# Kernel tuning notes

Hardware: AMD Instinct MI355X
Metric: run time of the kernel (lower is better)

Reference implementation:

```python
import jax, jax.numpy as jnp
import numpy as np

B = 64            # number of graphs
NODES_PER_G = 64  # real nodes per graph
N_MAX = 128       # max_num_nodes (dense padding)
NT = B * NODES_PER_G   # 4096 total nodes
E = 65536         # edges (and pairs)
H = 64            # hidden_dim
D_NODE = 32
POLY = 16


def setup_inputs() -> dict:
    key = jax.random.key(0)
    ks = jax.random.split(key, 12)
    node_x = jax.random.normal(ks[0], (NT, D_NODE), dtype=jnp.float32)
    loop_x = jax.random.normal(ks[1], (NT, POLY), dtype=jnp.float32)
    edge_attr = jax.random.normal(ks[2], (E, D_NODE), dtype=jnp.float32)
    pair_x = jax.random.normal(ks[3], (E, POLY), dtype=jnp.float32)
    W_node = jax.random.normal(ks[4], (D_NODE, H), dtype=jnp.float32) / np.sqrt(D_NODE)
    W_loop = jax.random.normal(ks[5], (POLY, H), dtype=jnp.float32) / np.sqrt(POLY)
    W_edge = jax.random.normal(ks[6], (D_NODE, H), dtype=jnp.float32) / np.sqrt(D_NODE)
    W_pair = jax.random.normal(ks[7], (POLY, H), dtype=jnp.float32) / np.sqrt(POLY)
    # sorted graph assignment: 64 nodes per graph
    batch = (jnp.arange(NT, dtype=jnp.int32) // NODES_PER_G).astype(jnp.int32)
    # intra-graph edges: global index = graph*NODES_PER_G + local
    epg = E // B  # edges per graph
    eg = (jnp.arange(E, dtype=jnp.int32) // epg)
    e_loc = jax.random.randint(ks[8], (2, E), 0, NODES_PER_G, dtype=jnp.int32)
    edge_index = eg[None, :] * NODES_PER_G + e_loc
    p_loc = jax.random.randint(ks[9], (2, E), 0, NODES_PER_G, dtype=jnp.int32)
    pair_index = eg[None, :] * NODES_PER_G + p_loc
    return {
        "node_x": node_x, "loop_x": loop_x, "edge_attr": edge_attr, "pair_x": pair_x,
        "W_node": W_node, "W_loop": W_loop, "W_edge": W_edge, "W_pair": W_pair,
        "batch": batch, "edge_index": edge_index, "pair_index": pair_index,
    }


def _positions(batch):
    # position of each node within its graph (to_dense_batch semantics)
    counts = jax.ops.segment_sum(jnp.ones_like(batch), batch, num_segments=B)
    starts = jnp.concatenate([jnp.zeros((1,), counts.dtype), jnp.cumsum(counts)[:-1]])
    return jnp.arange(batch.shape[0], dtype=batch.dtype) - starts[batch].astype(batch.dtype)


def _to_dense_adj(index, batch, pos, h):
    b = batch[index[0]]
    r = pos[index[0]]
    c = pos[index[1]]
    dense = jnp.zeros((B, N_MAX, N_MAX, H), dtype=h.dtype)
    return dense.at[b, r, c].add(h)  # duplicates are summed, as in to_dense_adj


def reference(node_x, loop_x, edge_attr, pair_x, W_node, W_loop, W_edge, W_pair,
              batch, edge_index, pair_index):
    pos = _positions(batch)
    # node + loop encoders (linear), then scatter to dense batch [B, N, H]
    node_h = node_x @ W_node + loop_x @ W_loop
    dense_node_h = jnp.zeros((B, N_MAX, H), dtype=node_h.dtype).at[batch, pos].set(node_h)
    dense_node_mask = jnp.zeros((B, N_MAX), dtype=bool).at[batch, pos].set(True)
    # permute (0,2,1) -> [B, H, N], then diag_embed -> [B, H, N, N]
    dnh = jnp.transpose(dense_node_h, (0, 2, 1))
    ar = jnp.arange(N_MAX)
    dense_diag_h = jnp.zeros((B, H, N_MAX, N_MAX), dtype=dnh.dtype).at[:, :, ar, ar].set(dnh)
    # edge + pair encoders, scatter to dense adjacency [B, N, N, H]
    edge_h = edge_attr @ W_edge
    pair_h = pair_x @ W_pair
    dense_pair = _to_dense_adj(edge_index, batch, pos, edge_h) \
               + _to_dense_adj(pair_index, batch, pos, pair_h)
    # permute (0,3,1,2) -> [B, H, N, N], add diagonal node features
    dense_pair_h = jnp.transpose(dense_pair, (0, 3, 1, 2)) + dense_diag_h
    return dense_pair_h, dense_node_mask
```

## Files before the change

### kernel.cpp

```cpp
#include <hip/hip_runtime.h>

#define NTOT  4096
#define NG    64
#define NMAXD 128
#define HD    64
#define NEDGE 65536
#define EPG   (NEDGE / NG)
#define NPG   (NTOT / NG)

typedef float f4 __attribute__((ext_vector_type(4)));

__global__ __launch_bounds__(1024) void prep_kernel(const int* __restrict__ batch,
                                                    int* __restrict__ starts,
                                                    int* __restrict__ pos,
                                                    int* __restrict__ counts) {
  const int tid = threadIdx.x;
  for (int i = tid; i < NTOT; i += 1024)
    if (i == 0 || batch[i] != batch[i - 1]) starts[batch[i]] = i;
  if (tid == 0) starts[NG] = NTOT;
  __syncthreads();
  for (int i = tid; i < NTOT; i += 1024) pos[i] = i - starts[batch[i]];
  if (tid < NG) counts[tid] = starts[tid + 1] - starts[tid];
}

#define HQ 4
#define SCT 512
__global__ __launch_bounds__(SCT) void fused_scatter_kernel(
    const float* __restrict__ node_x, const float* __restrict__ loop_x,
    const float* __restrict__ edge_attr, const float* __restrict__ pair_x,
    const float* __restrict__ Wn, const float* __restrict__ Wl,
    const float* __restrict__ We, const float* __restrict__ Wp,
    const int* __restrict__ eI, const int* __restrict__ pI,
    const int* __restrict__ batch, const int* __restrict__ pos,
    const int* __restrict__ counts,
    float* __restrict__ out, float* __restrict__ mask) {
  __shared__ float acc[HQ * 4096];
  __shared__ f4 WcE[32];
  __shared__ f4 WcP[16];
  __shared__ f4 WcN[48];

  const int tid = threadIdx.x;
  const int d  = (int)blockIdx.x;
  const int g  = ((d & 7) << 3) | ((d >> 3) & 7);
  const int h0 = (d >> 6) * HQ;

  if (tid < 32)       WcE[tid]            = *(const f4*)&We[tid * HD + h0];
  else if (tid < 48)  WcP[tid - 32]       = *(const f4*)&Wp[(tid - 32) * HD + h0];
  else if (tid < 80)  WcN[tid - 48]       = *(const f4*)&Wn[(tid - 48) * HD + h0];
  else if (tid < 96)  WcN[32 + tid - 80]  = *(const f4*)&Wl[(tid - 80) * HD + h0];
  for (int i = tid; i < HQ * 1024; i += SCT) ((f4*)acc)[i] = (f4)(0.f);
  __syncthreads();

  const int wid = tid >> 6;
  if (wid >= 4) {
    const int tz = tid - 256;
#pragma unroll
    for (int t = 0; t < HQ; ++t) {
      f4* plane = (f4*)(out + ((size_t)g * HD + h0 + t) * NMAXD * NMAXD);
#pragma unroll
      for (int k = 0; k < 4; ++k) {
        const int idx = tz + k * 256;
        const int r = idx >> 4, c4 = 16 + (idx & 15);
        plane[r * 32 + c4] = (f4)(0.f);
      }
#pragma unroll
      for (int k = 0; k < 8; ++k)
        plane[2048 + tz + k * 256] = (f4)(0.f);
    }
    if (h0 == 0) {
      const int cg = counts[g];
      for (int i = tz; i < NMAXD; i += 256)
        mask[(size_t)g * NMAXD + i] = (i < cg) ? 1.0f : 0.0f;
    }
  } else {
    const int la = tid;

    for (int jj = la; jj < EPG; jj += 256) {
      const int j = g * EPG + jj;
      const f4* xr = (const f4*)(edge_attr + (size_t)j * 32);
      f4 d4 = (f4)(0.f);
#pragma unroll
      for (int k4 = 0; k4 < 8; ++k4) {
        const f4 x = xr[k4];
#pragma unroll
        for (int u = 0; u < 4; ++u) d4 += x[u] * WcE[k4 * 4 + u];
      }
      const int n0 = eI[j], n1 = eI[NEDGE + j];
      const int b = batch[n0], r = pos[n0], c = pos[n1];
      if (b == g && r < 64 && c < 64) {
        const int a = r * 64 + c;
        atomicAdd(&acc[a], d4.x);          atomicAdd(&acc[4096 + a], d4.y);
        atomicAdd(&acc[8192 + a], d4.z);   atomicAdd(&acc[12288 + a], d4.w);
      } else {
        atomicAdd(&out[(((size_t)b * HD + h0 + 0) * NMAXD + r) * NMAXD + c], d4.x);
        atomicAdd(&out[(((size_t)b * HD + h0 + 1) * NMAXD + r) * NMAXD + c], d4.y);
        atomicAdd(&out[(((size_t)b * HD + h0 + 2) * NMAXD + r) * NMAXD + c], d4.z);
        atomicAdd(&out[(((size_t)b * HD + h0 + 3) * NMAXD + r) * NMAXD + c], d4.w);
      }
    }

    for (int jj = la; jj < EPG; jj += 256) {
      const int j = g * EPG + jj;
      const f4* xr = (const f4*)(pair_x + (size_t)j * 16);
      f4 d4 = (f4)(0.f);
#pragma unroll
      for (int k4 = 0; k4 < 4; ++k4) {
        const f4 x = xr[k4];
#pragma unroll
        for (int u = 0; u < 4; ++u) d4 += x[u] * WcP[k4 * 4 + u];
      }
      const int n0 = pI[j], n1 = pI[NEDGE + j];
      const int b = batch[n0], r = pos[n0], c = pos[n1];
      if (b == g && r < 64 && c < 64) {
        const int a = r * 64 + c;
        atomicAdd(&acc[a], d4.x);          atomicAdd(&acc[4096 + a], d4.y);
        atomicAdd(&acc[8192 + a], d4.z);   atomicAdd(&acc[12288 + a], d4.w);
      } else {
        atomicAdd(&out[(((size_t)b * HD + h0 + 0) * NMAXD + r) * NMAXD + c], d4.x);
        atomicAdd(&out[(((size_t)b * HD + h0 + 1) * NMAXD + r) * NMAXD + c], d4.y);
        atomicAdd(&out[(((size_t)b * HD + h0 + 2) * NMAXD + r) * NMAXD + c], d4.z);
        atomicAdd(&out[(((size_t)b * HD + h0 + 3) * NMAXD + r) * NMAXD + c], d4.w);
      }
    }

    for (int jj = la; jj < NPG; jj += 256) {
      const int j = g * NPG + jj;
      const f4* xr = (const f4*)(node_x + (size_t)j * 32);
      const f4* lr = (const f4*)(loop_x + (size_t)j * 16);
      f4 d4 = (f4)(0.f);
#pragma unroll
      for (int k4 = 0; k4 < 8; ++k4) {
        const f4 x = xr[k4];
#pragma unroll
        for (int u = 0; u < 4; ++u) d4 += x[u] * WcN[k4 * 4 + u];
      }
#pragma unroll
      for (int k4 = 0; k4 < 4; ++k4) {
        const f4 x = lr[k4];
#pragma unroll
        for (int u = 0; u < 4; ++u) d4 += x[u] * WcN[32 + k4 * 4 + u];
      }
      const int b = batch[j], r = pos[j];
      if (b == g && r < 64) {
        const int a = r * 64 + r;
        atomicAdd(&acc[a], d4.x);          atomicAdd(&acc[4096 + a], d4.y);
        atomicAdd(&acc[8192 + a], d4.z);   atomicAdd(&acc[12288 + a], d4.w);
      } else {
        atomicAdd(&out[(((size_t)b * HD + h0 + 0) * NMAXD + r) * NMAXD + r], d4.x);
        atomicAdd(&out[(((size_t)b * HD + h0 + 1) * NMAXD + r) * NMAXD + r], d4.y);
        atomicAdd(&out[(((size_t)b * HD + h0 + 2) * NMAXD + r) * NMAXD + r], d4.z);
        atomicAdd(&out[(((size_t)b * HD + h0 + 3) * NMAXD + r) * NMAXD + r], d4.w);
      }
    }
  }
  __syncthreads();

#pragma unroll
  for (int t = 0; t < HQ; ++t) {
    f4* plane = (f4*)(out + ((size_t)g * HD + h0 + t) * NMAXD * NMAXD);
#pragma unroll
    for (int k = 0; k < 2; ++k) {
      const int idx = tid + k * SCT;
      const int r = idx >> 4, c4 = idx & 15;
      plane[r * 32 + c4] = *(const f4*)&acc[t * 4096 + r * 64 + c4 * 4];
    }
  }
}

extern "C" void kernel_launch(void* const* d_in, const int* in_sizes, int n_in,
                              void* d_out, int out_size, void* d_ws, size_t ws_size,
                              hipStream_t stream) {
  const float* node_x    = (const float*)d_in[0];
  const float* loop_x    = (const float*)d_in[1];
  const float* edge_attr = (const float*)d_in[2];
  const float* pair_x    = (const float*)d_in[3];
  const float* W_node    = (const float*)d_in[4];
  const float* W_loop    = (const float*)d_in[5];
  const float* W_edge    = (const float*)d_in[6];
  const float* W_pair    = (const float*)d_in[7];
  const int*   batch     = (const int*)d_in[8];
  const int*   edge_index = (const int*)d_in[9];
  const int*   pair_index = (const int*)d_in[10];

  float* out  = (float*)d_out;
  float* mask = out + (size_t)NG * HD * NMAXD * NMAXD;

  int* pos    = (int*)d_ws;
  int* starts = pos + NTOT;
  int* counts = starts + (NG + 1);

  prep_kernel<<<1, 1024, 0, stream>>>(batch, starts, pos, counts);
  fused_scatter_kernel<<<NG * 16, SCT, 0, stream>>>(node_x, loop_x, edge_attr,
      pair_x, W_node, W_loop, W_edge, W_pair, edge_index, pair_index,
      batch, pos, counts, out, mask);
}
```

Baseline: 91.68 us.

## Split zero-fill into separate blocks so all scatter threads process edges

```diff
diff --git a/kernel.cpp b/kernel.cpp
--- a/kernel.cpp
+++ b/kernel.cpp
@@ -23,9 +23,12 @@
   if (tid < NG) counts[tid] = starts[tid + 1] - starts[tid];
 }
 
-#define HQ 4
-#define SCT 512
-__global__ __launch_bounds__(SCT) void fused_scatter_kernel(
+#define HQ  4
+#define BT  512
+#define NBB 1024
+#define NZB 1024
+
+__global__ __launch_bounds__(BT) void mega_kernel(
     const float* __restrict__ node_x, const float* __restrict__ loop_x,
     const float* __restrict__ edge_attr, const float* __restrict__ pair_x,
     const float* __restrict__ Wn, const float* __restrict__ Wl,
@@ -34,12 +37,29 @@
     const int* __restrict__ batch, const int* __restrict__ pos,
     const int* __restrict__ counts,
     float* __restrict__ out, float* __restrict__ mask) {
+  const int tid = threadIdx.x;
+
+  if ((int)blockIdx.x >= NBB) {
+    const int z = (int)blockIdx.x - NBB;
+#pragma unroll
+    for (int t = 0; t < 4; ++t) {
+      f4* plane = (f4*)(out + (size_t)(z * 4 + t) * (NMAXD * NMAXD));
+#pragma unroll
+      for (int k = 0; k < 4; ++k) plane[2048 + tid + k * BT] = (f4)(0.f);
+#pragma unroll
+      for (int k = 0; k < 2; ++k) {
+        const int i = tid + k * BT;
+        plane[(i >> 4) * 32 + 16 + (i & 15)] = (f4)(0.f);
+      }
+    }
+    return;
+  }
+
   __shared__ float acc[HQ * 4096];
   __shared__ f4 WcE[32];
   __shared__ f4 WcP[16];
   __shared__ f4 WcN[48];
 
-  const int tid = threadIdx.x;
   const int d  = (int)blockIdx.x;
   const int g  = ((d & 7) << 3) | ((d >> 3) & 7);
   const int h0 = (d >> 6) * HQ;
@@ -48,109 +68,84 @@
   else if (tid < 48)  WcP[tid - 32]       = *(const f4*)&Wp[(tid - 32) * HD + h0];
   else if (tid < 80)  WcN[tid - 48]       = *(const f4*)&Wn[(tid - 48) * HD + h0];
   else if (tid < 96)  WcN[32 + tid - 80]  = *(const f4*)&Wl[(tid - 80) * HD + h0];
-  for (int i = tid; i < HQ * 1024; i += SCT) ((f4*)acc)[i] = (f4)(0.f);
+  for (int i = tid; i < HQ * 1024; i += BT) ((f4*)acc)[i] = (f4)(0.f);
   __syncthreads();
 
-  const int wid = tid >> 6;
-  if (wid >= 4) {
-    const int tz = tid - 256;
+  for (int jj = tid; jj < EPG; jj += BT) {
+    const int j = g * EPG + jj;
+    const f4* xr = (const f4*)(edge_attr + (size_t)j * 32);
+    f4 d4 = (f4)(0.f);
 #pragma unroll
-    for (int t = 0; t < HQ; ++t) {
-      f4* plane = (f4*)(out + ((size_t)g * HD + h0 + t) * NMAXD * NMAXD);
+    for (int k4 = 0; k4 < 8; ++k4) {
+      const f4 x = xr[k4];
 #pragma unroll
-      for (int k = 0; k < 4; ++k) {
-        const int idx = tz + k * 256;
-        const int r = idx >> 4, c4 = 16 + (idx & 15);
-        plane[r * 32 + c4] = (f4)(0.f);
-      }
+      for (int u = 0; u < 4; ++u) d4 += x[u] * WcE[k4 * 4 + u];
+    }
+    const int n0 = eI[j], n1 = eI[NEDGE + j];
+    const int b = batch[n0], r = pos[n0], c = pos[n1];
+    if (b == g && r < 64 && c < 64) {
+      const int a = r * 64 + c;
+      atomicAdd(&acc[a], d4.x);          atomicAdd(&acc[4096 + a], d4.y);
+      atomicAdd(&acc[8192 + a], d4.z);   atomicAdd(&acc[12288 + a], d4.w);
+    } else {
+      atomicAdd(&out[(((size_t)b * HD + h0 + 0) * NMAXD + r) * NMAXD + c], d4.x);
+      atomicAdd(&out[(((size_t)b * HD + h0 + 1) * NMAXD + r) * NMAXD + c], d4.y);
+      atomicAdd(&out[(((size_t)b * HD + h0 + 2) * NMAXD + r) * NMAXD + c], d4.z);
+      atomicAdd(&out[(((size_t)b * HD + h0 + 3) * NMAXD + r) * NMAXD + c], d4.w);
+    }
+  }
+
+  for (int jj = tid; jj < EPG; jj += BT) {
+    const int j = g * EPG + jj;
+    const f4* xr = (const f4*)(pair_x + (size_t)j * 16);
+    f4 d4 = (f4)(0.f);
 #pragma unroll
-      for (int k = 0; k < 8; ++k)
-        plane[2048 + tz + k * 256] = (f4)(0.f);
+    for (int k4 = 0; k4 < 4; ++k4) {
+      const f4 x = xr[k4];
+#pragma unroll
+      for (int u = 0; u < 4; ++u) d4 += x[u] * WcP[k4 * 4 + u];
     }
-    if (h0 == 0) {
-      const int cg = counts[g];
-      for (int i = tz; i < NMAXD; i += 256)
-        mask[(size_t)g * NMAXD + i] = (i < cg) ? 1.0f : 0.0f;
+    const int n0 = pI[j], n1 = pI[NEDGE + j];
+    const int b = batch[n0], r = pos[n0], c = pos[n1];
+    if (b == g && r < 64 && c < 64) {
+      const int a = r * 64 + c;
+      atomicAdd(&acc[a], d4.x);          atomicAdd(&acc[4096 + a], d4.y);
+      atomicAdd(&acc[8192 + a], d4.z);   atomicAdd(&acc[12288 + a], d4.w);
+    } else {
+      atomicAdd(&out[(((size_t)b * HD + h0 + 0) * NMAXD + r) * NMAXD + c], d4.x);
+      atomicAdd(&out[(((size_t)b * HD + h0 + 1) * NMAXD + r) * NMAXD + c], d4.y);
+      atomicAdd(&out[(((size_t)b * HD + h0 + 2) * NMAXD + r) * NMAXD + c], d4.z);
+      atomicAdd(&out[(((size_t)b * HD + h0 + 3) * NMAXD + r) * NMAXD + c], d4.w);
     }
-  } else {
-    const int la = tid;
+  }
 
-    for (int jj = la; jj < EPG; jj += 256) {
-      const int j = g * EPG + jj;
-      const f4* xr = (const f4*)(edge_attr + (size_t)j * 32);
-      f4 d4 = (f4)(0.f);
+  if (tid < NPG) {
+    const int j = g * NPG + tid;
+    const f4* xr = (const f4*)(node_x + (size_t)j * 32);
+    const f4* lr = (const f4*)(loop_x + (size_t)j * 16);
+    f4 d4 = (f4)(0.f);
 #pragma unroll
-      for (int k4 = 0; k4 < 8; ++k4) {
-        const f4 x = xr[k4];
+    for (int k4 = 0; k4 < 8; ++k4) {
+      const f4 x = xr[k4];
 #pragma unroll
-        for (int u = 0; u < 4; ++u) d4 += x[u] * WcE[k4 * 4 + u];
-      }
-      const int n0 = eI[j], n1 = eI[NEDGE + j];
-      const int b = batch[n0], r = pos[n0], c = pos[n1];
-      if (b == g && r < 64 && c < 64) {
-        const int a = r * 64 + c;
-        atomicAdd(&acc[a], d4.x);          atomicAdd(&acc[4096 + a], d4.y);
-        atomicAdd(&acc[8192 + a], d4.z);   atomicAdd(&acc[12288 + a], d4.w);
-      } else {
-        atomicAdd(&out[(((size_t)b * HD + h0 + 0) * NMAXD + r) * NMAXD + c], d4.x);
-        atomicAdd(&out[(((size_t)b * HD + h0 + 1) * NMAXD + r) * NMAXD + c], d4.y);
-        atomicAdd(&out[(((size_t)b * HD + h0 + 2) * NMAXD + r) * NMAXD + c], d4.z);
-        atomicAdd(&out[(((size_t)b * HD + h0 + 3) * NMAXD + r) * NMAXD + c], d4.w);
-      }
+      for (int u = 0; u < 4; ++u) d4 += x[u] * WcN[k4 * 4 + u];
     }
-
-    for (int jj = la; jj < EPG; jj += 256) {
-      const int j = g * EPG + jj;
-      const f4* xr = (const f4*)(pair_x + (size_t)j * 16);
-      f4 d4 = (f4)(0.f);
 #pragma unroll
-      for (int k4 = 0; k4 < 4; ++k4) {
-        const f4 x = xr[k4];
+    for (int k4 = 0; k4 < 4; ++k4) {
+      const f4 x = lr[k4];
 #pragma unroll
-        for (int u = 0; u < 4; ++u) d4 += x[u] * WcP[k4 * 4 + u];
-      }
-      const int n0 = pI[j], n1 = pI[NEDGE + j];
-      const int b = batch[n0], r = pos[n0], c = pos[n1];
-      if (b == g && r < 64 && c < 64) {
-        const int a = r * 64 + c;
-        atomicAdd(&acc[a], d4.x);          atomicAdd(&acc[4096 + a], d4.y);
-        atomicAdd(&acc[8192 + a], d4.z);   atomicAdd(&acc[12288 + a], d4.w);
-      } else {
-        atomicAdd(&out[(((size_t)b * HD + h0 + 0) * NMAXD + r) * NMAXD + c], d4.x);
-        atomicAdd(&out[(((size_t)b * HD + h0 + 1) * NMAXD + r) * NMAXD + c], d4.y);
-        atomicAdd(&out[(((size_t)b * HD + h0 + 2) * NMAXD + r) * NMAXD + c], d4.z);
-        atomicAdd(&out[(((size_t)b * HD + h0 + 3) * NMAXD + r) * NMAXD + c], d4.w);
-      }
+      for (int u = 0; u < 4; ++u) d4 += x[u] * WcN[32 + k4 * 4 + u];
     }
-
-    for (int jj = la; jj < NPG; jj += 256) {
-      const int j = g * NPG + jj;
-      const f4* xr = (const f4*)(node_x + (size_t)j * 32);
-      const f4* lr = (const f4*)(loop_x + (size_t)j * 16);
-      f4 d4 = (f4)(0.f);
-#pragma unroll
-      for (int k4 = 0; k4 < 8; ++k4) {
-        const f4 x = xr[k4];
-#pragma unroll
-        for (int u = 0; u < 4; ++u) d4 += x[u] * WcN[k4 * 4 + u];
-      }
-#pragma unroll
-      for (int k4 = 0; k4 < 4; ++k4) {
-        const f4 x = lr[k4];
-#pragma unroll
-        for (int u = 0; u < 4; ++u) d4 += x[u] * WcN[32 + k4 * 4 + u];
-      }
-      const int b = batch[j], r = pos[j];
-      if (b == g && r < 64) {
-        const int a = r * 64 + r;
-        atomicAdd(&acc[a], d4.x);          atomicAdd(&acc[4096 + a], d4.y);
-        atomicAdd(&acc[8192 + a], d4.z);   atomicAdd(&acc[12288 + a], d4.w);
-      } else {
-        atomicAdd(&out[(((size_t)b * HD + h0 + 0) * NMAXD + r) * NMAXD + r], d4.x);
-        atomicAdd(&out[(((size_t)b * HD + h0 + 1) * NMAXD + r) * NMAXD + r], d4.y);
-        atomicAdd(&out[(((size_t)b * HD + h0 + 2) * NMAXD + r) * NMAXD + r], d4.z);
-        atomicAdd(&out[(((size_t)b * HD + h0 + 3) * NMAXD + r) * NMAXD + r], d4.w);
-      }
+    const int b = batch[j], r = pos[j];
+    if (b == g && r < 64) {
+      const int a = r * 64 + r;
+      atomicAdd(&acc[a], d4.x);          atomicAdd(&acc[4096 + a], d4.y);
+      atomicAdd(&acc[8192 + a], d4.z);   atomicAdd(&acc[12288 + a], d4.w);
+    } else {
+      atomicAdd(&out[(((size_t)b * HD + h0 + 0) * NMAXD + r) * NMAXD + r], d4.x);
+      atomicAdd(&out[(((size_t)b * HD + h0 + 1) * NMAXD + r) * NMAXD + r], d4.y);
+      atomicAdd(&out[(((size_t)b * HD + h0 + 2) * NMAXD + r) * NMAXD + r], d4.z);
+      atomicAdd(&out[(((size_t)b * HD + h0 + 3) * NMAXD + r) * NMAXD + r], d4.w);
     }
   }
   __syncthreads();
@@ -160,11 +155,14 @@
     f4* plane = (f4*)(out + ((size_t)g * HD + h0 + t) * NMAXD * NMAXD);
 #pragma unroll
     for (int k = 0; k < 2; ++k) {
-      const int idx = tid + k * SCT;
+      const int idx = tid + k * BT;
       const int r = idx >> 4, c4 = idx & 15;
       plane[r * 32 + c4] = *(const f4*)&acc[t * 4096 + r * 64 + c4 * 4];
     }
   }
+
+  if (h0 == 0 && tid < NMAXD)
+    mask[(size_t)g * NMAXD + tid] = (tid < counts[g]) ? 1.0f : 0.0f;
 }
 
 extern "C" void kernel_launch(void* const* d_in, const int* in_sizes, int n_in,
@@ -190,7 +188,7 @@
   int* counts = starts + (NG + 1);
 
   prep_kernel<<<1, 1024, 0, stream>>>(batch, starts, pos, counts);
-  fused_scatter_kernel<<<NG * 16, SCT, 0, stream>>>(node_x, loop_x, edge_attr,
+  mega_kernel<<<NBB + NZB, BT, 0, stream>>>(node_x, loop_x, edge_attr,
       pair_x, W_node, W_loop, W_edge, W_pair, edge_index, pair_index,
       batch, pos, counts, out, mask);
 }
```

Result: slower. 101.6 us (+10.8%).

## Precompute packed graph/row/col codes per edge and use unsafe atomics

Applied to the files above, without the earlier changes.

```diff
diff --git a/kernel.cpp b/kernel.cpp
--- a/kernel.cpp
+++ b/kernel.cpp
@@ -10,17 +10,37 @@
 
 typedef float f4 __attribute__((ext_vector_type(4)));
 
-__global__ __launch_bounds__(1024) void prep_kernel(const int* __restrict__ batch,
-                                                    int* __restrict__ starts,
-                                                    int* __restrict__ pos,
-                                                    int* __restrict__ counts) {
-  const int tid = threadIdx.x;
-  for (int i = tid; i < NTOT; i += 1024)
-    if (i == 0 || batch[i] != batch[i - 1]) starts[batch[i]] = i;
-  if (tid == 0) starts[NG] = NTOT;
-  __syncthreads();
-  for (int i = tid; i < NTOT; i += 1024) pos[i] = i - starts[batch[i]];
-  if (tid < NG) counts[tid] = starts[tid + 1] - starts[tid];
+__device__ __forceinline__ int lowb(const int* __restrict__ batch, int key) {
+  int lo = 0, hi = NTOT;
+  while (lo < hi) { const int mid = (lo + hi) >> 1;
+    if (batch[mid] < key) lo = mid + 1; else hi = mid; }
+  return lo;
+}
+
+__global__ __launch_bounds__(256) void prep_all_kernel(
+    const int* __restrict__ eI, const int* __restrict__ pI,
+    const int* __restrict__ batch,
+    int* __restrict__ rcE, int* __restrict__ rcP, int* __restrict__ rcN,
+    int* __restrict__ counts) {
+  const int i = blockIdx.x * 256 + threadIdx.x;
+  if (i < NEDGE) {
+    const int n0 = eI[i], n1 = eI[NEDGE + i];
+    const int b0 = batch[n0], b1 = batch[n1];
+    rcE[i] = (b0 << 16) | ((n0 - lowb(batch, b0)) << 8) | (n1 - lowb(batch, b1));
+  } else if (i < 2 * NEDGE) {
+    const int j = i - NEDGE;
+    const int n0 = pI[j], n1 = pI[NEDGE + j];
+    const int b0 = batch[n0], b1 = batch[n1];
+    rcP[j] = (b0 << 16) | ((n0 - lowb(batch, b0)) << 8) | (n1 - lowb(batch, b1));
+  } else if (i < 2 * NEDGE + NTOT) {
+    const int j = i - 2 * NEDGE;
+    const int b = batch[j];
+    const int p = j - lowb(batch, b);
+    rcN[j] = (b << 16) | (p << 8) | p;
+  } else if (i < 2 * NEDGE + NTOT + NG) {
+    const int g = i - 2 * NEDGE - NTOT;
+    counts[g] = lowb(batch, g + 1) - lowb(batch, g);
+  }
 }
 
 #define HQ 4
@@ -30,9 +50,8 @@
     const float* __restrict__ edge_attr, const float* __restrict__ pair_x,
     const float* __restrict__ Wn, const float* __restrict__ Wl,
     const float* __restrict__ We, const float* __restrict__ Wp,
-    const int* __restrict__ eI, const int* __restrict__ pI,
-    const int* __restrict__ batch, const int* __restrict__ pos,
-    const int* __restrict__ counts,
+    const int* __restrict__ rcE, const int* __restrict__ rcP,
+    const int* __restrict__ rcN, const int* __restrict__ counts,
     float* __restrict__ out, float* __restrict__ mask) {
   __shared__ float acc[HQ * 4096];
   __shared__ f4 WcE[32];
@@ -60,8 +79,7 @@
 #pragma unroll
       for (int k = 0; k < 4; ++k) {
         const int idx = tz + k * 256;
-        const int r = idx >> 4, c4 = 16 + (idx & 15);
-        plane[r * 32 + c4] = (f4)(0.f);
+        plane[(idx >> 4) * 32 + 16 + (idx & 15)] = (f4)(0.f);
       }
 #pragma unroll
       for (int k = 0; k < 8; ++k)
@@ -73,10 +91,9 @@
         mask[(size_t)g * NMAXD + i] = (i < cg) ? 1.0f : 0.0f;
     }
   } else {
-    const int la = tid;
-
-    for (int jj = la; jj < EPG; jj += 256) {
-      const int j = g * EPG + jj;
+#pragma unroll
+    for (int k = 0; k < 4; ++k) {
+      const int j = g * EPG + tid + k * 256;
       const f4* xr = (const f4*)(edge_attr + (size_t)j * 32);
       f4 d4 = (f4)(0.f);
 #pragma unroll
@@ -85,22 +102,23 @@
 #pragma unroll
         for (int u = 0; u < 4; ++u) d4 += x[u] * WcE[k4 * 4 + u];
       }
-      const int n0 = eI[j], n1 = eI[NEDGE + j];
-      const int b = batch[n0], r = pos[n0], c = pos[n1];
+      const int code = rcE[j];
+      const int b = code >> 16, r = (code >> 8) & 255, c = code & 255;
       if (b == g && r < 64 && c < 64) {
         const int a = r * 64 + c;
-        atomicAdd(&acc[a], d4.x);          atomicAdd(&acc[4096 + a], d4.y);
-        atomicAdd(&acc[8192 + a], d4.z);   atomicAdd(&acc[12288 + a], d4.w);
+        unsafeAtomicAdd(&acc[a], d4.x);          unsafeAtomicAdd(&acc[4096 + a], d4.y);
+        unsafeAtomicAdd(&acc[8192 + a], d4.z);   unsafeAtomicAdd(&acc[12288 + a], d4.w);
       } else {
-        atomicAdd(&out[(((size_t)b * HD + h0 + 0) * NMAXD + r) * NMAXD + c], d4.x);
-        atomicAdd(&out[(((size_t)b * HD + h0 + 1) * NMAXD + r) * NMAXD + c], d4.y);
-        atomicAdd(&out[(((size_t)b * HD + h0 + 2) * NMAXD + r) * NMAXD + c], d4.z);
-        atomicAdd(&out[(((size_t)b * HD + h0 + 3) * NMAXD + r) * NMAXD + c], d4.w);
-      }
-    }
-
-    for (int jj = la; jj < EPG; jj += 256) {
-      const int j = g * EPG + jj;
+        unsafeAtomicAdd(&out[(((size_t)b * HD + h0 + 0) * NMAXD + r) * NMAXD + c], d4.x);
+        unsafeAtomicAdd(&out[(((size_t)b * HD + h0 + 1) * NMAXD + r) * NMAXD + c], d4.y);
+        unsafeAtomicAdd(&out[(((size_t)b * HD + h0 + 2) * NMAXD + r) * NMAXD + c], d4.z);
+        unsafeAtomicAdd(&out[(((size_t)b * HD + h0 + 3) * NMAXD + r) * NMAXD + c], d4.w);
+      }
+    }
+
+#pragma unroll
+    for (int k = 0; k < 4; ++k) {
+      const int j = g * EPG + tid + k * 256;
       const f4* xr = (const f4*)(pair_x + (size_t)j * 16);
       f4 d4 = (f4)(0.f);
 #pragma unroll
@@ -109,22 +127,22 @@
 #pragma unroll
         for (int u = 0; u < 4; ++u) d4 += x[u] * WcP[k4 * 4 + u];
       }
-      const int n0 = pI[j], n1 = pI[NEDGE + j];
-      const int b = batch[n0], r = pos[n0], c = pos[n1];
+      const int code = rcP[j];
+      const int b = code >> 16, r = (code >> 8) & 255, c = code & 255;
       if (b == g && r < 64 && c < 64) {
         const int a = r * 64 + c;
-        atomicAdd(&acc[a], d4.x);          atomicAdd(&acc[4096 + a], d4.y);
-        atomicAdd(&acc[8192 + a], d4.z);   atomicAdd(&acc[12288 + a], d4.w);
+        unsafeAtomicAdd(&acc[a], d4.x);          unsafeAtomicAdd(&acc[4096 + a], d4.y);
+        unsafeAtomicAdd(&acc[8192 + a], d4.z);   unsafeAtomicAdd(&acc[12288 + a], d4.w);
       } else {
-        atomicAdd(&out[(((size_t)b * HD + h0 + 0) * NMAXD + r) * NMAXD + c], d4.x);
-        atomicAdd(&out[(((size_t)b * HD + h0 + 1) * NMAXD + r) * NMAXD + c], d4.y);
-        atomicAdd(&out[(((size_t)b * HD + h0 + 2) * NMAXD + r) * NMAXD + c], d4.z);
-        atomicAdd(&out[(((size_t)b * HD + h0 + 3) * NMAXD + r) * NMAXD + c], d4.w);
-      }
-    }
-
-    for (int jj = la; jj < NPG; jj += 256) {
-      const int j = g * NPG + jj;
+        unsafeAtomicAdd(&out[(((size_t)b * HD + h0 + 0) * NMAXD + r) * NMAXD + c], d4.x);
+        unsafeAtomicAdd(&out[(((size_t)b * HD + h0 + 1) * NMAXD + r) * NMAXD + c], d4.y);
+        unsafeAtomicAdd(&out[(((size_t)b * HD + h0 + 2) * NMAXD + r) * NMAXD + c], d4.z);
+        unsafeAtomicAdd(&out[(((size_t)b * HD + h0 + 3) * NMAXD + r) * NMAXD + c], d4.w);
+      }
+    }
+
+    if (tid < NPG) {
+      const int j = g * NPG + tid;
       const f4* xr = (const f4*)(node_x + (size_t)j * 32);
       const f4* lr = (const f4*)(loop_x + (size_t)j * 16);
       f4 d4 = (f4)(0.f);
@@ -140,16 +158,17 @@
 #pragma unroll
         for (int u = 0; u < 4; ++u) d4 += x[u] * WcN[32 + k4 * 4 + u];
       }
-      const int b = batch[j], r = pos[j];
-      if (b == g && r < 64) {
-        const int a = r * 64 + r;
-        atomicAdd(&acc[a], d4.x);          atomicAdd(&acc[4096 + a], d4.y);
-        atomicAdd(&acc[8192 + a], d4.z);   atomicAdd(&acc[12288 + a], d4.w);
+      const int code = rcN[j];
+      const int b = code >> 16, r = (code >> 8) & 255, c = code & 255;
+      if (b == g && r < 64 && c < 64) {
+        const int a = r * 64 + c;
+        unsafeAtomicAdd(&acc[a], d4.x);          unsafeAtomicAdd(&acc[4096 + a], d4.y);
+        unsafeAtomicAdd(&acc[8192 + a], d4.z);   unsafeAtomicAdd(&acc[12288 + a], d4.w);
       } else {
-        atomicAdd(&out[(((size_t)b * HD + h0 + 0) * NMAXD + r) * NMAXD + r], d4.x);
-        atomicAdd(&out[(((size_t)b * HD + h0 + 1) * NMAXD + r) * NMAXD + r], d4.y);
-        atomicAdd(&out[(((size_t)b * HD + h0 + 2) * NMAXD + r) * NMAXD + r], d4.z);
-        atomicAdd(&out[(((size_t)b * HD + h0 + 3) * NMAXD + r) * NMAXD + r], d4.w);
+        unsafeAtomicAdd(&out[(((size_t)b * HD + h0 + 0) * NMAXD + r) * NMAXD + c], d4.x);
+        unsafeAtomicAdd(&out[(((size_t)b * HD + h0 + 1) * NMAXD + r) * NMAXD + c], d4.y);
+        unsafeAtomicAdd(&out[(((size_t)b * HD + h0 + 2) * NMAXD + r) * NMAXD + c], d4.z);
+        unsafeAtomicAdd(&out[(((size_t)b * HD + h0 + 3) * NMAXD + r) * NMAXD + c], d4.w);
       }
     }
   }
@@ -185,12 +204,14 @@
   float* out  = (float*)d_out;
   float* mask = out + (size_t)NG * HD * NMAXD * NMAXD;
 
-  int* pos    = (int*)d_ws;
-  int* starts = pos + NTOT;
-  int* counts = starts + (NG + 1);
-
-  prep_kernel<<<1, 1024, 0, stream>>>(batch, starts, pos, counts);
+  int* rcE    = (int*)d_ws;
+  int* rcP    = rcE + NEDGE;
+  int* rcN    = rcP + NEDGE;
+  int* counts = rcN + NTOT;
+
+  const int prep_items = 2 * NEDGE + NTOT + NG;
+  prep_all_kernel<<<(prep_items + 255) / 256, 256, 0, stream>>>(
+      edge_index, pair_index, batch, rcE, rcP, rcN, counts);
   fused_scatter_kernel<<<NG * 16, SCT, 0, stream>>>(node_x, loop_x, edge_attr,
-      pair_x, W_node, W_loop, W_edge, W_pair, edge_index, pair_index,
-      batch, pos, counts, out, mask);
-}
+      pair_x, W_node, W_loop, W_edge, W_pair, rcE, rcP, rcN, counts, out, mask);
+}
```

Result: faster. 73.39 us (-19.9%).
